# Kernel tuning notes

Measured on AMD Instinct MI355X. Metric: run time of the kernel, lower is better.

## Reference

```python
import jax, jax.numpy as jnp
import numpy as np

G, N, F, H, L, B = 8, 1024, 128, 256, 4, 64


def setup_inputs() -> dict:
    key = jax.random.key(0)
    ks = jax.random.split(key, 8)
    graph = jax.random.randint(ks[0], (B,), 0, G)
    # boolean coverpoint mask; force column 0 True so no row is empty
    mask = jax.random.uniform(ks[1], (B, N)) < 0.2
    mask = mask.at[:, 0].set(True)
    cdfg_xs = jax.random.normal(ks[2], (G, N, F), dtype=jnp.float32)
    cdfg_as = (jax.random.uniform(ks[3], (G, N, N)) < 0.02).astype(jnp.float32) / 20.0
    W_in = jax.random.normal(ks[4], (F, H), dtype=jnp.float32) * (1.0 / np.sqrt(F))
    b_in = jnp.zeros((H,), dtype=jnp.float32)
    Ws = jax.random.normal(ks[5], (L, H, H), dtype=jnp.float32) * (1.0 / np.sqrt(H))
    bs = jnp.zeros((L, H), dtype=jnp.float32)
    return {"graph": graph, "coverpoint_mask": mask, "cdfg_xs": cdfg_xs,
            "cdfg_as": cdfg_as, "W_in": W_in, "b_in": b_in, "Ws": Ws, "bs": bs}


def reference(graph, coverpoint_mask, cdfg_xs, cdfg_as, W_in, b_in, Ws, bs):
    # gather per-sample graphs (tf.gather_nd equivalent)
    xs = cdfg_xs[graph]          # [B, N, F]
    As = cdfg_as[graph]          # [B, N, N]
    # input Dense with relu
    x = jax.nn.relu(jnp.einsum('bnf,fh->bnh', xs, W_in) + b_in)  # [B, N, H]
    to_add = x
    n_layers = Ws.shape[0]
    for i in range(n_layers):
        h = jnp.einsum('bnm,bmh->bnh', As, jnp.einsum('bnh,hk->bnk', x, Ws[i])) + bs[i]
        if i == n_layers - 1:
            x = jax.nn.softmax(h, axis=-1)   # final_activation='softmax'
        else:
            x = jax.nn.relu(h)
    x = x + to_add
    # ragged boolean_mask + reduce_mean over nodes == masked mean
    m = coverpoint_mask[..., None].astype(x.dtype)   # [B, N, 1]
    s = jnp.sum(x * m, axis=1)                       # [B, H]
    cnt = jnp.maximum(jnp.sum(m, axis=1), 1.0)
    return s / cnt
```

## Files before the change

### kernel.cpp

```cpp
#include <hip/hip_runtime.h>
#include <hip/hip_bf16.h>

#define GG 8
#define NN 1024
#define FF 128
#define HH 256
#define LL 4
#define BB 64
#define MM (GG * NN)
#define ELLCAP 96

typedef __attribute__((ext_vector_type(8))) short bf16x8_t;
typedef __attribute__((ext_vector_type(4))) float f32x4_t;

__device__ inline unsigned short f2bf(float f) {
  union { float f; unsigned u; } c;
  c.f = f;
  unsigned r = (c.u + 0x7fffu + ((c.u >> 16) & 1u)) >> 16;
  return (unsigned short)r;
}
__device__ inline float bf2f(unsigned short u) {
  union { unsigned u; float f; } c;
  c.u = (unsigned)u << 16;
  return c.f;
}

__global__ __launch_bounds__(256) void prep_kernel(
    const uint4* __restrict__ mask4, int* __restrict__ flags,
    const float4* __restrict__ xs4, ushort4* __restrict__ xsb4,
    const float* __restrict__ W_in, const float* __restrict__ Ws,
    unsigned short* __restrict__ WinT, unsigned short* __restrict__ WsT,
    const float* __restrict__ Adj, uint2* __restrict__ ell,
    int* __restrict__ cntArr) {
  const int bx = blockIdx.x;
  const int t = threadIdx.x;
  if (bx == 0) {
    __shared__ int df[2];
    if (t < 2) df[t] = 0;
    __syncthreads();
    int nonz = 0, isf = 0;
    for (int i = t; i < 4096; i += 256) {
      const uint4 v = mask4[i];
      const unsigned all = v.x | v.y | v.z | v.w;
      if (all & 0xFFFFFF00u) nonz = 1;
      if (((v.x >> 24) == 0x3fu) || ((v.y >> 24) == 0x3fu) ||
          ((v.z >> 24) == 0x3fu) || ((v.w >> 24) == 0x3fu))
        isf = 1;
    }
    if (nonz) atomicOr(&df[0], 1);
    if (isf) atomicOr(&df[1], 1);
    __syncthreads();
    if (t == 0) flags[0] = df[1] ? 2 : (df[0] ? 0 : 1);
  } else if (bx < 1025) {
    const int i = (bx - 1) * 256 + t;
    const float4 v = xs4[i];
    ushort4 o;
    o.x = f2bf(v.x); o.y = f2bf(v.y); o.z = f2bf(v.z); o.w = f2bf(v.w);
    xsb4[i] = o;
  } else if (bx < 2177) {
    const int idx = (bx - 1025) * 256 + t;
    if (idx < FF * HH) {
      const int n = idx >> 7, k = idx & (FF - 1);
      WinT[idx] = f2bf(W_in[k * HH + n]);
    } else {
      const int j = idx - FF * HH;
      const int l = j >> 16, n = (j >> 8) & 255, k = j & 255;
      WsT[j] = f2bf(Ws[((size_t)l * HH + k) * HH + n]);
    }
  } else {
    const int lane = t & 63;
    const int wid = t >> 6;
    const int r = (bx - 2177) * 4 + wid;
    const float* __restrict__ Arow = Adj + (size_t)r * NN;
    int cnt = 0;
    for (int mc = 0; mc < NN; mc += 64) {
      const float a = Arow[mc + lane];
      const unsigned long long bal = __ballot(a != 0.0f);
      if (a != 0.0f) {
        const int pos = cnt + __popcll(bal & ((1ULL << lane) - 1ULL));
        if (pos < ELLCAP) {
          uint2 e;
          e.x = __float_as_uint(a);
          e.y = (unsigned)(mc + lane);
          ell[(size_t)r * ELLCAP + pos] = e;
        }
      }
      cnt += __popcll(bal);
    }
    if (lane == 0) cntArr[r] = min(cnt, ELLCAP);
  }
}

__global__ __launch_bounds__(256) void input_gemm_kernel(
    const unsigned short* __restrict__ A, const unsigned short* __restrict__ BT,
    const float* __restrict__ bias, unsigned short* __restrict__ Cb,
    float* __restrict__ Cf) {
  constexpr int K = FF, KS = K / 8;
  __shared__ uint4 As4[64 * KS];
  __shared__ uint4 Bs4[64 * KS];
  const int t = threadIdx.x;
  const int lane = t & 63;
  const int w = t >> 6;
  const int wm = (w >> 1) * 32;
  const int wn = (w & 1) * 32;
  const int m0 = blockIdx.x * 64;
  const int n0 = blockIdx.y * 64;
  const int lk = lane >> 4;
  const int lr = lane & 15;
  const uint4* __restrict__ Ag = (const uint4*)(A + (size_t)m0 * K);
  const uint4* __restrict__ Bg = (const uint4*)(BT + (size_t)n0 * K);
#pragma unroll
  for (int it = 0; it < K / 32; ++it) {
    const int c = it * 256 + t;
    const int row = c / KS;
    const int k = c % KS;
    const int slot = row * KS + (k ^ (row & 7));
    As4[slot] = Ag[c];
    Bs4[slot] = Bg[c];
  }
  __syncthreads();
  f32x4_t acc[2][2] = {};
#pragma unroll
  for (int ks = 0; ks < K / 32; ++ks) {
    const int q = ks * 4 + lk;
    const int ra0 = wm + lr, ra1 = wm + 16 + lr;
    const int rb0 = wn + lr, rb1 = wn + 16 + lr;
    const bf16x8_t a0 = *(const bf16x8_t*)(&As4[ra0 * KS + (q ^ (ra0 & 7))]);
    const bf16x8_t a1 = *(const bf16x8_t*)(&As4[ra1 * KS + (q ^ (ra1 & 7))]);
    const bf16x8_t b0 = *(const bf16x8_t*)(&Bs4[rb0 * KS + (q ^ (rb0 & 7))]);
    const bf16x8_t b1 = *(const bf16x8_t*)(&Bs4[rb1 * KS + (q ^ (rb1 & 7))]);
    acc[0][0] = __builtin_amdgcn_mfma_f32_16x16x32_bf16(a0, b0, acc[0][0], 0, 0, 0);
    acc[0][1] = __builtin_amdgcn_mfma_f32_16x16x32_bf16(a0, b1, acc[0][1], 0, 0, 0);
    acc[1][0] = __builtin_amdgcn_mfma_f32_16x16x32_bf16(a1, b0, acc[1][0], 0, 0, 0);
    acc[1][1] = __builtin_amdgcn_mfma_f32_16x16x32_bf16(a1, b1, acc[1][1], 0, 0, 0);
  }
#pragma unroll
  for (int rg = 0; rg < 2; ++rg)
#pragma unroll
    for (int cg = 0; cg < 2; ++cg)
#pragma unroll
      for (int j = 0; j < 4; ++j) {
        const int row = m0 + wm + rg * 16 + (lane >> 4) * 4 + j;
        const int col = n0 + wn + cg * 16 + lr;
        float v = acc[rg][cg][j] + bias[col];
        v = fmaxf(v, 0.0f);
        Cb[(size_t)row * HH + col] = f2bf(v);
        Cf[(size_t)row * HH + col] = v;
      }
}

template <bool FINAL>
__global__ __launch_bounds__(256) void layer_kernel(
    const uint2* __restrict__ ell, const int* __restrict__ cntArr,
    const unsigned short* __restrict__ Xin, const unsigned short* __restrict__ WT,
    const float* __restrict__ bias, unsigned short* __restrict__ Xout,
    float* __restrict__ Hout) {
  __shared__ __align__(16) unsigned short Z[16][264];
  __shared__ uint4 Wl[256 * 8];
  const int t = threadIdx.x;
  const int lane = t & 63;
  const int w = t >> 6;
  const int r0 = blockIdx.x * 16;
  const int g = r0 >> 10;
  const unsigned short* __restrict__ Xg = Xin + (size_t)g * NN * HH;

  for (int rr = w * 4; rr < w * 4 + 4; ++rr) {
    const int r = r0 + rr;
    const int cnt = cntArr[r];
    const uint2* __restrict__ erow = ell + (size_t)r * ELLCAP;
    float p0 = 0.f, p1 = 0.f, p2 = 0.f, p3 = 0.f;
    float q0 = 0.f, q1 = 0.f, q2 = 0.f, q3 = 0.f;
    for (int base = 0; base < cnt; base += 64) {
      const int m = min(64, cnt - base);
      const uint2 e = erow[base + ((lane < m) ? lane : 0)];
      int j = 0;
      for (; j + 2 <= m; j += 2) {
        const float v0 = __uint_as_float(__shfl(e.x, j));
        const int i0 = (int)__shfl(e.y, j);
        const float v1 = __uint_as_float(__shfl(e.x, j + 1));
        const int i1 = (int)__shfl(e.y, j + 1);
        const ushort4 y0 = *(const ushort4*)(Xg + (size_t)i0 * HH + (lane << 2));
        const ushort4 y1 = *(const ushort4*)(Xg + (size_t)i1 * HH + (lane << 2));
        p0 += v0 * bf2f(y0.x); p1 += v0 * bf2f(y0.y);
        p2 += v0 * bf2f(y0.z); p3 += v0 * bf2f(y0.w);
        q0 += v1 * bf2f(y1.x); q1 += v1 * bf2f(y1.y);
        q2 += v1 * bf2f(y1.z); q3 += v1 * bf2f(y1.w);
      }
      if (j < m) {
        const float v0 = __uint_as_float(__shfl(e.x, j));
        const int i0 = (int)__shfl(e.y, j);
        const ushort4 y0 = *(const ushort4*)(Xg + (size_t)i0 * HH + (lane << 2));
        p0 += v0 * bf2f(y0.x); p1 += v0 * bf2f(y0.y);
        p2 += v0 * bf2f(y0.z); p3 += v0 * bf2f(y0.w);
      }
    }
    ushort4 z;
    z.x = f2bf(p0 + q0); z.y = f2bf(p1 + q1);
    z.z = f2bf(p2 + q2); z.w = f2bf(p3 + q3);
    *(ushort4*)&Z[rr][lane << 2] = z;
  }
  __syncthreads();

  const int lr = lane & 15;
  const int lk = lane >> 4;
  f32x4_t acc[4] = {};
  for (int kc = 0; kc < 4; ++kc) {
    if (kc) __syncthreads();
#pragma unroll
    for (int it = 0; it < 8; ++it) {
      const int c = it * 256 + t;
      const int n = c >> 3, k8 = c & 7;
      Wl[n * 8 + (k8 ^ (n & 7))] = ((const uint4*)WT)[n * 32 + kc * 8 + k8];
    }
    __syncthreads();
#pragma unroll
    for (int ks = 0; ks < 2; ++ks) {
      const bf16x8_t a = *(const bf16x8_t*)&Z[lr][kc * 64 + ks * 32 + lk * 8];
      const int k8 = ks * 4 + lk;
#pragma unroll
      for (int nt = 0; nt < 4; ++nt) {
        const int n = w * 64 + nt * 16 + lr;
        const bf16x8_t b = *(const bf16x8_t*)&Wl[n * 8 + (k8 ^ (n & 7))];
        acc[nt] = __builtin_amdgcn_mfma_f32_16x16x32_bf16(a, b, acc[nt], 0, 0, 0);
      }
    }
  }
#pragma unroll
  for (int nt = 0; nt < 4; ++nt)
#pragma unroll
    for (int j = 0; j < 4; ++j) {
      const int row = r0 + lk * 4 + j;
      const int col = w * 64 + nt * 16 + lr;
      const float v = acc[nt][j] + bias[col];
      if (FINAL)
        Hout[(size_t)row * HH + col] = v;
      else
        Xout[(size_t)row * HH + col] = f2bf(fmaxf(v, 0.0f));
    }
}

__global__ __launch_bounds__(256) void softmax_res_kernel(
    const float* __restrict__ H, const float* __restrict__ X0,
    float* __restrict__ X) {
  const int lane = threadIdx.x & 63;
  const int wid = threadIdx.x >> 6;
  const int r = blockIdx.x * 4 + wid;
  const size_t rowoff = (size_t)r * HH;
  const float4 h4 = *(const float4*)(H + rowoff + (lane << 2));
  const float h0 = h4.x, h1 = h4.y, h2 = h4.z, h3 = h4.w;
  float mx = fmaxf(fmaxf(h0, h1), fmaxf(h2, h3));
#pragma unroll
  for (int off = 32; off >= 1; off >>= 1) mx = fmaxf(mx, __shfl_xor(mx, off));
  const float e0 = __expf(h0 - mx), e1 = __expf(h1 - mx);
  const float e2 = __expf(h2 - mx), e3 = __expf(h3 - mx);
  float s = e0 + e1 + e2 + e3;
#pragma unroll
  for (int off = 32; off >= 1; off >>= 1) s += __shfl_xor(s, off);
  const float inv = 1.0f / s;
  const float4 x0 = *(const float4*)(X0 + rowoff + (lane << 2));
  float4 o;
  o.x = e0 * inv + x0.x;
  o.y = e1 * inv + x0.y;
  o.z = e2 * inv + x0.z;
  o.w = e3 * inv + x0.w;
  *(float4*)(X + rowoff + (lane << 2)) = o;
}

__global__ __launch_bounds__(256) void mm_partial_kernel(
    const float* __restrict__ X, const int* __restrict__ graph,
    const void* __restrict__ mask, const int* __restrict__ flags,
    float* __restrict__ partial, float* __restrict__ cntbuf) {
  __shared__ unsigned char m[64];
  const int c = blockIdx.x;
  const int b = blockIdx.y;
  const int h = threadIdx.x;
  const int n0 = c * 64;
  const int mode = flags[0];
  if (h < 64) {
    const int n = n0 + h;
    bool on;
    if (mode == 1) on = ((const int*)mask)[(size_t)b * NN + n] != 0;
    else if (mode == 2) on = ((const float*)mask)[(size_t)b * NN + n] != 0.0f;
    else on = ((const unsigned char*)mask)[(size_t)b * NN + n] != 0;
    m[h] = on ? 1 : 0;
  }
  __syncthreads();
  const int g = graph[b];
  const float* __restrict__ Xg = X + ((size_t)g * NN + n0) * HH;
  float a0 = 0.f, a1 = 0.f, a2 = 0.f, a3 = 0.f;
  int c0 = 0, c1 = 0, c2 = 0, c3 = 0;
#pragma unroll 4
  for (int n = 0; n < 16; ++n) {
    if (m[n])      { a0 += Xg[(size_t)n * HH + h]; c0++; }
    if (m[n + 16]) { a1 += Xg[(size_t)(n + 16) * HH + h]; c1++; }
    if (m[n + 32]) { a2 += Xg[(size_t)(n + 32) * HH + h]; c2++; }
    if (m[n + 48]) { a3 += Xg[(size_t)(n + 48) * HH + h]; c3++; }
  }
  partial[((size_t)b * 16 + c) * HH + h] = (a0 + a1) + (a2 + a3);
  if (h == 0) cntbuf[b * 16 + c] = (float)((c0 + c1) + (c2 + c3));
}

__global__ __launch_bounds__(256) void mm_reduce_kernel(
    const float* __restrict__ partial, const float* __restrict__ cntbuf,
    float* __restrict__ out) {
  const int b = blockIdx.x, h = threadIdx.x;
  float s = 0.f;
#pragma unroll
  for (int c = 0; c < 16; ++c) s += partial[((size_t)b * 16 + c) * HH + h];
  float cnt = 0.f;
#pragma unroll
  for (int c = 0; c < 16; ++c) cnt += cntbuf[b * 16 + c];
  out[(size_t)b * HH + h] = s / fmaxf(cnt, 1.0f);
}

extern "C" void kernel_launch(void* const* d_in, const int* in_sizes, int n_in,
                              void* d_out, int out_size, void* d_ws,
                              size_t ws_size, hipStream_t stream) {
  const int* graph = (const int*)d_in[0];
  const void* mask = d_in[1];
  const float* xs = (const float*)d_in[2];
  const float* As = (const float*)d_in[3];
  const float* W_in = (const float*)d_in[4];
  const float* b_in = (const float*)d_in[5];
  const float* Ws = (const float*)d_in[6];
  const float* bs = (const float*)d_in[7];
  float* out = (float*)d_out;

  float* X = (float*)d_ws;
  float* X0 = X + (size_t)MM * HH;
  unsigned short* Yb = (unsigned short*)(X0 + (size_t)MM * HH);
  unsigned short* Xb = Yb + (size_t)MM * HH;
  unsigned short* xsb = Xb + (size_t)MM * HH;
  unsigned short* WinT = xsb + (size_t)MM * FF;
  unsigned short* WsT = WinT + (size_t)HH * FF;
  uint2* ell = (uint2*)(WsT + (size_t)LL * HH * HH);
  int* cntArr = (int*)(ell + (size_t)MM * ELLCAP);
  int* flags = cntArr + MM;
  float* partial = (float*)(flags + 2);
  float* cntbuf = partial + (size_t)BB * 16 * HH;

  prep_kernel<<<4225, 256, 0, stream>>>((const uint4*)mask, flags,
                                        (const float4*)xs, (ushort4*)xsb, W_in,
                                        Ws, WinT, WsT, As, ell, cntArr);
  input_gemm_kernel<<<dim3(MM / 64, HH / 64), 256, 0, stream>>>(xsb, WinT, b_in,
                                                                Xb, X0);
  layer_kernel<false><<<MM / 16, 256, 0, stream>>>(ell, cntArr, Xb, WsT, bs, Yb,
                                                   nullptr);
  layer_kernel<false><<<MM / 16, 256, 0, stream>>>(
      ell, cntArr, Yb, WsT + (size_t)HH * HH, bs + HH, Xb, nullptr);
  layer_kernel<false><<<MM / 16, 256, 0, stream>>>(
      ell, cntArr, Xb, WsT + (size_t)2 * HH * HH, bs + 2 * HH, Yb, nullptr);
  layer_kernel<true><<<MM / 16, 256, 0, stream>>>(
      ell, cntArr, Yb, WsT + (size_t)3 * HH * HH, bs + 3 * HH, nullptr, X);
  softmax_res_kernel<<<MM / 4, 256, 0, stream>>>(X, X0, X);
  mm_partial_kernel<<<dim3(16, BB), 256, 0, stream>>>(X, graph, mask, flags,
                                                      partial, cntbuf);
  mm_reduce_kernel<<<BB, 256, 0, stream>>>(partial, cntbuf, out);
}
```

Baseline: 222.6 us.

## Reorder layers to GEMM-then-SpMM, fuse softmax, restructure masked mean per graph

Each layer now computes X·W as a dense MFMA GEMM first and then aggregates with the ELL sparse adjacency, replacing the fused SpMM-then-GEMM kernel. The last layer's softmax and residual add are fused into the SpMM epilogue. The input GEMM is merged with ELL construction into one launch. Weight transposes go through LDS tiles for coalesced access, and the masked mean stages each graph's node chunk in shared memory once for all samples of that graph. This adds launches per layer and an extra bf16 intermediate round trip, in exchange for a cleaner GEMM and less redundant work.

```diff
diff --git a/kernel.cpp b/kernel.cpp
--- a/kernel.cpp
+++ b/kernel.cpp
@@ -9,6 +9,7 @@
 #define BB 64
 #define MM (GG * NN)
 #define ELLCAP 96
+#define NC 32
 
 typedef __attribute__((ext_vector_type(8))) short bf16x8_t;
 typedef __attribute__((ext_vector_type(4))) float f32x4_t;
@@ -29,13 +30,12 @@
     const uint4* __restrict__ mask4, int* __restrict__ flags,
     const float4* __restrict__ xs4, ushort4* __restrict__ xsb4,
     const float* __restrict__ W_in, const float* __restrict__ Ws,
-    unsigned short* __restrict__ WinT, unsigned short* __restrict__ WsT,
-    const float* __restrict__ Adj, uint2* __restrict__ ell,
-    int* __restrict__ cntArr) {
+    unsigned short* __restrict__ WinT, unsigned short* __restrict__ WsT) {
+  __shared__ float Ld[64][65];
+  __shared__ int df[2];
   const int bx = blockIdx.x;
   const int t = threadIdx.x;
   if (bx == 0) {
-    __shared__ int df[2];
     if (t < 2) df[t] = 0;
     __syncthreads();
     int nonz = 0, isf = 0;
@@ -57,20 +57,99 @@
     ushort4 o;
     o.x = f2bf(v.x); o.y = f2bf(v.y); o.z = f2bf(v.z); o.w = f2bf(v.w);
     xsb4[i] = o;
-  } else if (bx < 2177) {
-    const int idx = (bx - 1025) * 256 + t;
-    if (idx < FF * HH) {
-      const int n = idx >> 7, k = idx & (FF - 1);
-      WinT[idx] = f2bf(W_in[k * HH + n]);
+  } else {
+    int tt = bx - 1025;
+    const float* src;
+    unsigned short* dst;
+    int R, C, r0, c0;
+    if (tt < 8) {
+      src = W_in; dst = WinT; R = FF; C = HH;
+      r0 = (tt >> 2) * 64; c0 = (tt & 3) * 64;
     } else {
-      const int j = idx - FF * HH;
-      const int l = j >> 16, n = (j >> 8) & 255, k = j & 255;
-      WsT[j] = f2bf(Ws[((size_t)l * HH + k) * HH + n]);
-    }
+      tt -= 8;
+      const int l = tt >> 4, rem = tt & 15;
+      src = Ws + (size_t)l * HH * HH;
+      dst = WsT + (size_t)l * HH * HH;
+      R = HH; C = HH;
+      r0 = (rem >> 2) * 64; c0 = (rem & 3) * 64;
+    }
+#pragma unroll
+    for (int i = 0; i < 16; ++i) {
+      const int idx = i * 256 + t;
+      const int r = idx >> 6, c = idx & 63;
+      Ld[r][c] = src[(size_t)(r0 + r) * C + c0 + c];
+    }
+    __syncthreads();
+#pragma unroll
+    for (int i = 0; i < 16; ++i) {
+      const int idx = i * 256 + t;
+      const int cc = idx >> 6, rr = idx & 63;
+      dst[(size_t)(c0 + cc) * R + r0 + rr] = f2bf(Ld[rr][cc]);
+    }
+  }
+}
+
+__global__ __launch_bounds__(256) void stage2_kernel(
+    const unsigned short* __restrict__ A, const unsigned short* __restrict__ BT,
+    const float* __restrict__ bias, unsigned short* __restrict__ Cb,
+    float* __restrict__ Cf, const float* __restrict__ Adj,
+    uint2* __restrict__ ell, int* __restrict__ cntArr) {
+  constexpr int K = FF, KS = K / 8;
+  __shared__ uint4 As4[64 * KS];
+  __shared__ uint4 Bs4[64 * KS];
+  const int bx = blockIdx.x;
+  const int t = threadIdx.x;
+  const int lane = t & 63;
+  const int w = t >> 6;
+  if (bx < 512) {
+    const int wm = (w >> 1) * 32;
+    const int wn = (w & 1) * 32;
+    const int m0 = (bx >> 2) * 64;
+    const int n0 = (bx & 3) * 64;
+    const int lk = lane >> 4;
+    const int lr = lane & 15;
+    const uint4* __restrict__ Ag = (const uint4*)(A + (size_t)m0 * K);
+    const uint4* __restrict__ Bg = (const uint4*)(BT + (size_t)n0 * K);
+#pragma unroll
+    for (int it = 0; it < K / 32; ++it) {
+      const int c = it * 256 + t;
+      const int row = c / KS;
+      const int k = c % KS;
+      const int slot = row * KS + (k ^ (row & 7));
+      As4[slot] = Ag[c];
+      Bs4[slot] = Bg[c];
+    }
+    __syncthreads();
+    f32x4_t acc[2][2] = {};
+#pragma unroll
+    for (int ks = 0; ks < K / 32; ++ks) {
+      const int q = ks * 4 + lk;
+      const int ra0 = wm + lr, ra1 = wm + 16 + lr;
+      const int rb0 = wn + lr, rb1 = wn + 16 + lr;
+      const bf16x8_t a0 = *(const bf16x8_t*)(&As4[ra0 * KS + (q ^ (ra0 & 7))]);
+      const bf16x8_t a1 = *(const bf16x8_t*)(&As4[ra1 * KS + (q ^ (ra1 & 7))]);
+      const bf16x8_t b0 = *(const bf16x8_t*)(&Bs4[rb0 * KS + (q ^ (rb0 & 7))]);
+      const bf16x8_t b1 = *(const bf16x8_t*)(&Bs4[rb1 * KS + (q ^ (rb1 & 7))]);
+      acc[0][0] = __builtin_amdgcn_mfma_f32_16x16x32_bf16(a0, b0, acc[0][0], 0, 0, 0);
+      acc[0][1] = __builtin_amdgcn_mfma_f32_16x16x32_bf16(a0, b1, acc[0][1], 0, 0, 0);
+      acc[1][0] = __builtin_amdgcn_mfma_f32_16x16x32_bf16(a1, b0, acc[1][0], 0, 0, 0);
+      acc[1][1] = __builtin_amdgcn_mfma_f32_16x16x32_bf16(a1, b1, acc[1][1], 0, 0, 0);
+    }
+#pragma unroll
+    for (int rg = 0; rg < 2; ++rg)
+#pragma unroll
+      for (int cg = 0; cg < 2; ++cg)
+#pragma unroll
+        for (int j = 0; j < 4; ++j) {
+          const int row = m0 + wm + rg * 16 + (lane >> 4) * 4 + j;
+          const int col = n0 + wn + cg * 16 + lr;
+          float v = acc[rg][cg][j] + bias[col];
+          v = fmaxf(v, 0.0f);
+          Cb[(size_t)row * HH + col] = f2bf(v);
+          Cf[(size_t)row * HH + col] = v;
+        }
   } else {
-    const int lane = t & 63;
-    const int wid = t >> 6;
-    const int r = (bx - 2177) * 4 + wid;
+    const int r = (bx - 512) * 4 + w;
     const float* __restrict__ Arow = Adj + (size_t)r * NN;
     int cnt = 0;
     for (int mc = 0; mc < NN; mc += 64) {
@@ -91,11 +170,10 @@
   }
 }
 
-__global__ __launch_bounds__(256) void input_gemm_kernel(
+__global__ __launch_bounds__(256) void layer_gemm_kernel(
     const unsigned short* __restrict__ A, const unsigned short* __restrict__ BT,
-    const float* __restrict__ bias, unsigned short* __restrict__ Cb,
-    float* __restrict__ Cf) {
-  constexpr int K = FF, KS = K / 8;
+    unsigned short* __restrict__ Cb) {
+  constexpr int K = HH, KS = K / 8;
   __shared__ uint4 As4[64 * KS];
   __shared__ uint4 Bs4[64 * KS];
   const int t = threadIdx.x;
@@ -142,162 +220,118 @@
       for (int j = 0; j < 4; ++j) {
         const int row = m0 + wm + rg * 16 + (lane >> 4) * 4 + j;
         const int col = n0 + wn + cg * 16 + lr;
-        float v = acc[rg][cg][j] + bias[col];
-        v = fmaxf(v, 0.0f);
-        Cb[(size_t)row * HH + col] = f2bf(v);
-        Cf[(size_t)row * HH + col] = v;
+        Cb[(size_t)row * HH + col] = f2bf(acc[rg][cg][j]);
       }
 }
 
-template <bool FINAL>
-__global__ __launch_bounds__(256) void layer_kernel(
+__global__ __launch_bounds__(256) void spmm_ell_kernel(
     const uint2* __restrict__ ell, const int* __restrict__ cntArr,
-    const unsigned short* __restrict__ Xin, const unsigned short* __restrict__ WT,
-    const float* __restrict__ bias, unsigned short* __restrict__ Xout,
-    float* __restrict__ Hout) {
-  __shared__ __align__(16) unsigned short Z[16][264];
-  __shared__ uint4 Wl[256 * 8];
-  const int t = threadIdx.x;
-  const int lane = t & 63;
-  const int w = t >> 6;
-  const int r0 = blockIdx.x * 16;
-  const int g = r0 >> 10;
-  const unsigned short* __restrict__ Xg = Xin + (size_t)g * NN * HH;
-
-  for (int rr = w * 4; rr < w * 4 + 4; ++rr) {
-    const int r = r0 + rr;
-    const int cnt = cntArr[r];
-    const uint2* __restrict__ erow = ell + (size_t)r * ELLCAP;
-    float p0 = 0.f, p1 = 0.f, p2 = 0.f, p3 = 0.f;
-    float q0 = 0.f, q1 = 0.f, q2 = 0.f, q3 = 0.f;
-    for (int base = 0; base < cnt; base += 64) {
-      const int m = min(64, cnt - base);
-      const uint2 e = erow[base + ((lane < m) ? lane : 0)];
-      int j = 0;
-      for (; j + 2 <= m; j += 2) {
-        const float v0 = __uint_as_float(__shfl(e.x, j));
-        const int i0 = (int)__shfl(e.y, j);
-        const float v1 = __uint_as_float(__shfl(e.x, j + 1));
-        const int i1 = (int)__shfl(e.y, j + 1);
-        const ushort4 y0 = *(const ushort4*)(Xg + (size_t)i0 * HH + (lane << 2));
-        const ushort4 y1 = *(const ushort4*)(Xg + (size_t)i1 * HH + (lane << 2));
-        p0 += v0 * bf2f(y0.x); p1 += v0 * bf2f(y0.y);
-        p2 += v0 * bf2f(y0.z); p3 += v0 * bf2f(y0.w);
-        q0 += v1 * bf2f(y1.x); q1 += v1 * bf2f(y1.y);
-        q2 += v1 * bf2f(y1.z); q3 += v1 * bf2f(y1.w);
-      }
-      if (j < m) {
-        const float v0 = __uint_as_float(__shfl(e.x, j));
-        const int i0 = (int)__shfl(e.y, j);
-        const ushort4 y0 = *(const ushort4*)(Xg + (size_t)i0 * HH + (lane << 2));
-        p0 += v0 * bf2f(y0.x); p1 += v0 * bf2f(y0.y);
-        p2 += v0 * bf2f(y0.z); p3 += v0 * bf2f(y0.w);
-      }
-    }
-    ushort4 z;
-    z.x = f2bf(p0 + q0); z.y = f2bf(p1 + q1);
-    z.z = f2bf(p2 + q2); z.w = f2bf(p3 + q3);
-    *(ushort4*)&Z[rr][lane << 2] = z;
-  }
-  __syncthreads();
-
-  const int lr = lane & 15;
-  const int lk = lane >> 4;
-  f32x4_t acc[4] = {};
-  for (int kc = 0; kc < 4; ++kc) {
-    if (kc) __syncthreads();
-#pragma unroll
-    for (int it = 0; it < 8; ++it) {
-      const int c = it * 256 + t;
-      const int n = c >> 3, k8 = c & 7;
-      Wl[n * 8 + (k8 ^ (n & 7))] = ((const uint4*)WT)[n * 32 + kc * 8 + k8];
-    }
-    __syncthreads();
-#pragma unroll
-    for (int ks = 0; ks < 2; ++ks) {
-      const bf16x8_t a = *(const bf16x8_t*)&Z[lr][kc * 64 + ks * 32 + lk * 8];
-      const int k8 = ks * 4 + lk;
-#pragma unroll
-      for (int nt = 0; nt < 4; ++nt) {
-        const int n = w * 64 + nt * 16 + lr;
-        const bf16x8_t b = *(const bf16x8_t*)&Wl[n * 8 + (k8 ^ (n & 7))];
-        acc[nt] = __builtin_amdgcn_mfma_f32_16x16x32_bf16(a, b, acc[nt], 0, 0, 0);
-      }
-    }
-  }
-#pragma unroll
-  for (int nt = 0; nt < 4; ++nt)
-#pragma unroll
-    for (int j = 0; j < 4; ++j) {
-      const int row = r0 + lk * 4 + j;
-      const int col = w * 64 + nt * 16 + lr;
-      const float v = acc[nt][j] + bias[col];
-      if (FINAL)
-        Hout[(size_t)row * HH + col] = v;
-      else
-        Xout[(size_t)row * HH + col] = f2bf(fmaxf(v, 0.0f));
-    }
-}
-
-__global__ __launch_bounds__(256) void softmax_res_kernel(
-    const float* __restrict__ H, const float* __restrict__ X0,
-    float* __restrict__ X) {
+    const unsigned short* __restrict__ Yb, const float* __restrict__ bias,
+    const float* __restrict__ X0, unsigned short* __restrict__ Xb,
+    float* __restrict__ Xf, int final_layer) {
   const int lane = threadIdx.x & 63;
   const int wid = threadIdx.x >> 6;
   const int r = blockIdx.x * 4 + wid;
+  const int g = r >> 10;
+  const unsigned short* __restrict__ Yg = Yb + (size_t)g * NN * HH;
+  const int cnt = cntArr[r];
+  const uint2* __restrict__ erow = ell + (size_t)r * ELLCAP;
+  float p0 = 0.f, p1 = 0.f, p2 = 0.f, p3 = 0.f;
+  float q0 = 0.f, q1 = 0.f, q2 = 0.f, q3 = 0.f;
+  for (int base = 0; base < cnt; base += 64) {
+    const int m = min(64, cnt - base);
+    const uint2 e = erow[base + ((lane < m) ? lane : 0)];
+    int j = 0;
+    for (; j + 2 <= m; j += 2) {
+      const float v0 = __uint_as_float(__shfl(e.x, j));
+      const int i0 = (int)__shfl(e.y, j);
+      const float v1 = __uint_as_float(__shfl(e.x, j + 1));
+      const int i1 = (int)__shfl(e.y, j + 1);
+      const ushort4 y0 = *(const ushort4*)(Yg + (size_t)i0 * HH + (lane << 2));
+      const ushort4 y1 = *(const ushort4*)(Yg + (size_t)i1 * HH + (lane << 2));
+      p0 += v0 * bf2f(y0.x); p1 += v0 * bf2f(y0.y);
+      p2 += v0 * bf2f(y0.z); p3 += v0 * bf2f(y0.w);
+      q0 += v1 * bf2f(y1.x); q1 += v1 * bf2f(y1.y);
+      q2 += v1 * bf2f(y1.z); q3 += v1 * bf2f(y1.w);
+    }
+    if (j < m) {
+      const float v0 = __uint_as_float(__shfl(e.x, j));
+      const int i0 = (int)__shfl(e.y, j);
+      const ushort4 y0 = *(const ushort4*)(Yg + (size_t)i0 * HH + (lane << 2));
+      p0 += v0 * bf2f(y0.x); p1 += v0 * bf2f(y0.y);
+      p2 += v0 * bf2f(y0.z); p3 += v0 * bf2f(y0.w);
+    }
+  }
+  const float4 b4 = *(const float4*)(bias + (lane << 2));
+  const float h0 = p0 + q0 + b4.x, h1 = p1 + q1 + b4.y;
+  const float h2 = p2 + q2 + b4.z, h3 = p3 + q3 + b4.w;
   const size_t rowoff = (size_t)r * HH;
-  const float4 h4 = *(const float4*)(H + rowoff + (lane << 2));
-  const float h0 = h4.x, h1 = h4.y, h2 = h4.z, h3 = h4.w;
-  float mx = fmaxf(fmaxf(h0, h1), fmaxf(h2, h3));
-#pragma unroll
-  for (int off = 32; off >= 1; off >>= 1) mx = fmaxf(mx, __shfl_xor(mx, off));
-  const float e0 = __expf(h0 - mx), e1 = __expf(h1 - mx);
-  const float e2 = __expf(h2 - mx), e3 = __expf(h3 - mx);
-  float s = e0 + e1 + e2 + e3;
-#pragma unroll
-  for (int off = 32; off >= 1; off >>= 1) s += __shfl_xor(s, off);
-  const float inv = 1.0f / s;
-  const float4 x0 = *(const float4*)(X0 + rowoff + (lane << 2));
-  float4 o;
-  o.x = e0 * inv + x0.x;
-  o.y = e1 * inv + x0.y;
-  o.z = e2 * inv + x0.z;
-  o.w = e3 * inv + x0.w;
-  *(float4*)(X + rowoff + (lane << 2)) = o;
+  if (!final_layer) {
+    ushort4 o;
+    o.x = f2bf(fmaxf(h0, 0.f));
+    o.y = f2bf(fmaxf(h1, 0.f));
+    o.z = f2bf(fmaxf(h2, 0.f));
+    o.w = f2bf(fmaxf(h3, 0.f));
+    *(ushort4*)(Xb + rowoff + (lane << 2)) = o;
+  } else {
+    float mx = fmaxf(fmaxf(h0, h1), fmaxf(h2, h3));
+#pragma unroll
+    for (int off = 32; off >= 1; off >>= 1) mx = fmaxf(mx, __shfl_xor(mx, off));
+    const float e0 = __expf(h0 - mx), e1 = __expf(h1 - mx);
+    const float e2 = __expf(h2 - mx), e3 = __expf(h3 - mx);
+    float s = e0 + e1 + e2 + e3;
+#pragma unroll
+    for (int off = 32; off >= 1; off >>= 1) s += __shfl_xor(s, off);
+    const float inv = 1.0f / s;
+    const float4 x0 = *(const float4*)(X0 + rowoff + (lane << 2));
+    float4 o;
+    o.x = e0 * inv + x0.x;
+    o.y = e1 * inv + x0.y;
+    o.z = e2 * inv + x0.z;
+    o.w = e3 * inv + x0.w;
+    *(float4*)(Xf + rowoff + (lane << 2)) = o;
+  }
 }
 
 __global__ __launch_bounds__(256) void mm_partial_kernel(
     const float* __restrict__ X, const int* __restrict__ graph,
     const void* __restrict__ mask, const int* __restrict__ flags,
     float* __restrict__ partial, float* __restrict__ cntbuf) {
-  __shared__ unsigned char m[64];
+  __shared__ float Xl[32][256];
   const int c = blockIdx.x;
-  const int b = blockIdx.y;
-  const int h = threadIdx.x;
-  const int n0 = c * 64;
+  const int g = blockIdx.y;
+  const int t = threadIdx.x;
+  const int n0 = c * 32;
+  const float* __restrict__ Xg = X + ((size_t)g * NN + n0) * HH;
+#pragma unroll
+  for (int i = 0; i < 8; ++i) {
+    const int fidx = i * 256 + t;
+    const int row = fidx >> 6, c4 = fidx & 63;
+    *(float4*)&Xl[row][c4 << 2] =
+        *(const float4*)(Xg + (size_t)row * HH + (c4 << 2));
+  }
+  __syncthreads();
   const int mode = flags[0];
-  if (h < 64) {
-    const int n = n0 + h;
-    bool on;
-    if (mode == 1) on = ((const int*)mask)[(size_t)b * NN + n] != 0;
-    else if (mode == 2) on = ((const float*)mask)[(size_t)b * NN + n] != 0.0f;
-    else on = ((const unsigned char*)mask)[(size_t)b * NN + n] != 0;
-    m[h] = on ? 1 : 0;
-  }
-  __syncthreads();
-  const int g = graph[b];
-  const float* __restrict__ Xg = X + ((size_t)g * NN + n0) * HH;
-  float a0 = 0.f, a1 = 0.f, a2 = 0.f, a3 = 0.f;
-  int c0 = 0, c1 = 0, c2 = 0, c3 = 0;
-#pragma unroll 4
-  for (int n = 0; n < 16; ++n) {
-    if (m[n])      { a0 += Xg[(size_t)n * HH + h]; c0++; }
-    if (m[n + 16]) { a1 += Xg[(size_t)(n + 16) * HH + h]; c1++; }
-    if (m[n + 32]) { a2 += Xg[(size_t)(n + 32) * HH + h]; c2++; }
-    if (m[n + 48]) { a3 += Xg[(size_t)(n + 48) * HH + h]; c3++; }
-  }
-  partial[((size_t)b * 16 + c) * HH + h] = (a0 + a1) + (a2 + a3);
-  if (h == 0) cntbuf[b * 16 + c] = (float)((c0 + c1) + (c2 + c3));
+  for (int b = 0; b < BB; ++b) {
+    if (graph[b] != g) continue;
+    float a = 0.f;
+    int cnt = 0;
+    if (mode == 0) {
+      const unsigned char* mb = (const unsigned char*)mask + (size_t)b * NN + n0;
+      for (int n = 0; n < 32; ++n)
+        if (mb[n]) { a += Xl[n][t]; cnt++; }
+    } else if (mode == 1) {
+      const int* mi = (const int*)mask + (size_t)b * NN + n0;
+      for (int n = 0; n < 32; ++n)
+        if (mi[n] != 0) { a += Xl[n][t]; cnt++; }
+    } else {
+      const float* mf = (const float*)mask + (size_t)b * NN + n0;
+      for (int n = 0; n < 32; ++n)
+        if (mf[n] != 0.0f) { a += Xl[n][t]; cnt++; }
+    }
+    partial[((size_t)b * NC + c) * HH + t] = a;
+    if (t == 0) cntbuf[b * NC + c] = (float)cnt;
+  }
 }
 
 __global__ __launch_bounds__(256) void mm_reduce_kernel(
@@ -306,10 +340,10 @@
   const int b = blockIdx.x, h = threadIdx.x;
   float s = 0.f;
 #pragma unroll
-  for (int c = 0; c < 16; ++c) s += partial[((size_t)b * 16 + c) * HH + h];
+  for (int c = 0; c < NC; ++c) s += partial[((size_t)b * NC + c) * HH + h];
   float cnt = 0.f;
 #pragma unroll
-  for (int c = 0; c < 16; ++c) cnt += cntbuf[b * 16 + c];
+  for (int c = 0; c < NC; ++c) cnt += cntbuf[b * NC + c];
   out[(size_t)b * HH + h] = s / fmaxf(cnt, 1.0f);
 }
 
@@ -337,23 +371,20 @@
   int* cntArr = (int*)(ell + (size_t)MM * ELLCAP);
   int* flags = cntArr + MM;
   float* partial = (float*)(flags + 2);
-  float* cntbuf = partial + (size_t)BB * 16 * HH;
-
-  prep_kernel<<<4225, 256, 0, stream>>>((const uint4*)mask, flags,
+  float* cntbuf = partial + (size_t)BB * NC * HH;
+
+  prep_kernel<<<1097, 256, 0, stream>>>((const uint4*)mask, flags,
                                         (const float4*)xs, (ushort4*)xsb, W_in,
-                                        Ws, WinT, WsT, As, ell, cntArr);
-  input_gemm_kernel<<<dim3(MM / 64, HH / 64), 256, 0, stream>>>(xsb, WinT, b_in,
-                                                                Xb, X0);
-  layer_kernel<false><<<MM / 16, 256, 0, stream>>>(ell, cntArr, Xb, WsT, bs, Yb,
-                                                   nullptr);
-  layer_kernel<false><<<MM / 16, 256, 0, stream>>>(
-      ell, cntArr, Yb, WsT + (size_t)HH * HH, bs + HH, Xb, nullptr);
-  layer_kernel<false><<<MM / 16, 256, 0, stream>>>(
-      ell, cntArr, Xb, WsT + (size_t)2 * HH * HH, bs + 2 * HH, Yb, nullptr);
-  layer_kernel<true><<<MM / 16, 256, 0, stream>>>(
-      ell, cntArr, Yb, WsT + (size_t)3 * HH * HH, bs + 3 * HH, nullptr, X);
-  softmax_res_kernel<<<MM / 4, 256, 0, stream>>>(X, X0, X);
-  mm_partial_kernel<<<dim3(16, BB), 256, 0, stream>>>(X, graph, mask, flags,
+                                        Ws, WinT, WsT);
+  stage2_kernel<<<2560, 256, 0, stream>>>(xsb, WinT, b_in, Xb, X0, As, ell,
+                                          cntArr);
+  for (int i = 0; i < LL; ++i) {
+    layer_gemm_kernel<<<dim3(MM / 64, HH / 64), 256, 0, stream>>>(
+        Xb, WsT + (size_t)i * HH * HH, Yb);
+    spmm_ell_kernel<<<MM / 4, 256, 0, stream>>>(
+        ell, cntArr, Yb, bs + (size_t)i * HH, X0, Xb, X, (i == LL - 1) ? 1 : 0);
+  }
+  mm_partial_kernel<<<dim3(NC, GG), 256, 0, stream>>>(X, graph, mask, flags,
                                                       partial, cntbuf);
   mm_reduce_kernel<<<BB, 256, 0, stream>>>(partial, cntbuf, out);
 }
```

Result: faster. 211.4 us (-5.1%).
